# Kernel tuning notes

Hardware: AMD Instinct MI355X
Metric: run time of the kernel (lower is better)

Reference implementation:

```python
import jax, jax.numpy as jnp
import numpy as np
import math

B, L, H, NH = 8, 512, 512, 8
DH = H // NH


def setup_inputs() -> dict:
    key = jax.random.key(0)
    ks = jax.random.split(key, 12)
    src = jax.random.normal(ks[0], (B, L, H), dtype=jnp.float32)
    seq_len = jax.random.randint(ks[1], (B,), L // 2, L + 1).astype(jnp.int32)
    seq_len = seq_len.at[0].set(L)  # guarantee max(seq_len) == L
    pe = jax.random.normal(ks[2], (2 * L, H), dtype=jnp.float32) * 0.02
    s = 1.0 / math.sqrt(H)
    Wq = jax.random.normal(ks[3], (H, H), dtype=jnp.float32) * s
    bq = jnp.zeros((H,), jnp.float32)
    Wk = jax.random.normal(ks[4], (H, H), dtype=jnp.float32) * s
    bk = jnp.zeros((H,), jnp.float32)
    Wv = jax.random.normal(ks[5], (H, H), dtype=jnp.float32) * s
    bv = jnp.zeros((H,), jnp.float32)
    Wr = jax.random.normal(ks[6], (H, H), dtype=jnp.float32) * s
    br = jnp.zeros((H,), jnp.float32)
    u = jax.random.normal(ks[7], (NH, DH), dtype=jnp.float32) * 0.02
    v = jax.random.normal(ks[8], (NH, DH), dtype=jnp.float32) * 0.02
    gamma = jnp.ones((H,), jnp.float32)
    beta = jnp.zeros((H,), jnp.float32)
    return dict(src=src, seq_len=seq_len, pe=pe, Wq=Wq, bq=bq, Wk=Wk, bk=bk,
                Wv=Wv, bv=bv, Wr=Wr, br=br, u=u, v=v, gamma=gamma, beta=beta)


def reference(src, seq_len, pe, Wq, bq, Wk, bk, Wv, bv, Wr, br, u, v, gamma, beta):
    b, l, h = src.shape
    dh = h // NH
    # relative distance rel[i,j] = j - i, lookup pe[rel + L]  -> [L, L, H]
    rel = jnp.arange(l)[None, :] - jnp.arange(l)[:, None]
    R = pe[rel + l]
    # projections (torch Linear: y = x W^T + b)
    q = src @ Wq.T + bq
    k = src @ Wk.T + bk
    val = src @ Wv.T + bv
    R = R @ Wr.T + br
    # split heads
    q = q.reshape(b, l, NH, dh)
    k = k.reshape(b, l, NH, dh)
    val = val.reshape(b, l, NH, dh)
    R = R.reshape(l, l, NH, dh)
    # Transformer-XL score terms
    A = jnp.einsum('bihd,bjhd->bhij', q, k)
    Bt = jnp.einsum('bihd,ijhd->bhij', q, R)
    C = jnp.einsum('hd,bjhd->bhj', u, k)[:, :, None, :]
    D = jnp.einsum('ijhd,hd->hij', R, v)[None]
    scores = (A + Bt + C + D) / math.sqrt(dh)
    # key-side padding mask
    mask = jnp.arange(l)[None, :] < seq_len[:, None]  # [B, L]
    scores = jnp.where(mask[:, None, None, :], scores, jnp.float32(-1e15))
    attn = jax.nn.softmax(scores, axis=-1)
    out = jnp.einsum('bhij,bjhd->bihd', attn, val).reshape(b, l, h)
    res = src + out
    # LayerNorm (eps=1e-5) then exact GELU
    mu = jnp.mean(res, axis=-1, keepdims=True)
    var = jnp.mean((res - mu) ** 2, axis=-1, keepdims=True)
    ln = (res - mu) * jax.lax.rsqrt(var + 1e-5) * gamma + beta
    return jax.nn.gelu(ln, approximate=False)
```

## Files before the change

kernel.cpp:

```cpp
#include <hip/hip_runtime.h>
#include <math.h>

#define Bn 8
#define Ln 512
#define Hn 512
#define NHn 8
#define DHn 64

typedef __attribute__((ext_vector_type(8))) short short8;
typedef __attribute__((ext_vector_type(4))) float f32x4;

__device__ __forceinline__ unsigned short f2bf(float f) {
    unsigned int u = __float_as_uint(f);
    unsigned int r = (u + 0x7FFFu + ((u >> 16) & 1u)) >> 16;
    return (unsigned short)r;
}
__device__ __forceinline__ float bf2f(unsigned short s) {
    return __uint_as_float(((unsigned int)s) << 16);
}

__device__ __forceinline__ void gload16(const unsigned short* g, unsigned short* l) {
    __builtin_amdgcn_global_load_lds(
        (const __attribute__((address_space(1))) unsigned int*)g,
        (__attribute__((address_space(3))) unsigned int*)l, 16, 0, 0);
}

__global__ __launch_bounds__(256) void convert_kernel(
    const float* __restrict__ src, const float* __restrict__ pe,
    const float* __restrict__ Wq, const float* __restrict__ Wk,
    const float* __restrict__ Wv, const float* __restrict__ Wr,
    const float* __restrict__ bq, const float* __restrict__ bk,
    const float* __restrict__ bv,
    unsigned short* __restrict__ src_bf, unsigned short* __restrict__ pe_bf,
    unsigned short* __restrict__ Wcat_bf, unsigned short* __restrict__ Wr_bf,
    float* __restrict__ bcat)
{
    const int bid = blockIdx.x;
    const int tid = threadIdx.x;
    const float* in; unsigned short* outp; int base4;
    if (bid < 2048)      { in = src; outp = src_bf;           base4 = bid; }
    else if (bid < 2560) { in = pe;  outp = pe_bf;            base4 = bid - 2048; }
    else if (bid < 2816) { in = Wq;  outp = Wcat_bf;          base4 = bid - 2560; }
    else if (bid < 3072) { in = Wk;  outp = Wcat_bf + 262144; base4 = bid - 2816; }
    else if (bid < 3328) { in = Wv;  outp = Wcat_bf + 524288; base4 = bid - 3072; }
    else if (bid < 3584) { in = Wr;  outp = Wr_bf;            base4 = bid - 3328; }
    else {
        const int idx = (bid - 3584) * 256 + tid;
        if (idx < 512)            bcat[idx] = bq[idx];
        else if (idx < 1024)      bcat[idx] = bk[idx - 512];
        else if (idx < 1536)      bcat[idx] = bv[idx - 1024];
        return;
    }
    const int i4 = (base4 * 256 + tid) * 4;
    float4 x = *(const float4*)&in[i4];
    ushort4 o;
    o.x = f2bf(x.x); o.y = f2bf(x.y); o.z = f2bf(x.z); o.w = f2bf(x.w);
    *(ushort4*)&outp[i4] = o;
}

__global__ __launch_bounds__(256) void gemm_kernel(
    const unsigned short* __restrict__ src_bf,
    const unsigned short* __restrict__ Wcat_bf,
    const unsigned short* __restrict__ pe_bf,
    const unsigned short* __restrict__ Wr_bf,
    const float* __restrict__ bcat, const float* __restrict__ br,
    unsigned short* __restrict__ QKb,
    unsigned short* __restrict__ VTg,
    unsigned short* __restrict__ Rpb)
{
    const int bid = blockIdx.x;
    int mode, m0, n0;
    const unsigned short *A, *B;
    if (bid < 512) {
        mode = 0; m0 = (bid >> 3) * 64; n0 = (bid & 7) * 128;
        A = src_bf + (size_t)m0 * 512;
        B = Wcat_bf + (size_t)n0 * 512;
    } else if (bid < 768) {
        const int idx = bid - 512;
        mode = 1; m0 = (idx & 7) * 64; n0 = (idx >> 3) * 128;
        A = Wcat_bf + (size_t)(1024 + m0) * 512;
        B = src_bf + (size_t)n0 * 512;
    } else {
        const int idx = bid - 768;
        mode = 2; m0 = (idx >> 2) * 64; n0 = (idx & 3) * 128;
        A = pe_bf + (size_t)m0 * 512;
        B = Wr_bf + (size_t)n0 * 512;
    }

    __shared__ unsigned short lds[2][12288];

    const int t = threadIdx.x;
    const int wave = t >> 6, lane = t & 63;
    const int wm = (wave >> 1) * 32;
    const int wn = (wave & 1) * 64;
    const int l = lane & 15, g = lane >> 4;

    f32x4 acc[2][4] = {};

    const int lrow = lane >> 3;
    const int lcol = ((lane & 7) ^ lrow) * 8;
    const unsigned short* Ag0 = A + (size_t)((wave * 2 + 0) * 8 + lrow) * 512 + lcol;
    const unsigned short* Ag1 = A + (size_t)((wave * 2 + 1) * 8 + lrow) * 512 + lcol;
    const unsigned short* Bg0 = B + (size_t)((wave * 4 + 0) * 8 + lrow) * 512 + lcol;
    const unsigned short* Bg1 = B + (size_t)((wave * 4 + 1) * 8 + lrow) * 512 + lcol;
    const unsigned short* Bg2 = B + (size_t)((wave * 4 + 2) * 8 + lrow) * 512 + lcol;
    const unsigned short* Bg3 = B + (size_t)((wave * 4 + 3) * 8 + lrow) * 512 + lcol;

    const int aB0 = (wave * 2 + 0) * 512;
    const int aB1 = (wave * 2 + 1) * 512;
    const int bB0 = 4096 + (wave * 4 + 0) * 512;
    const int bB1 = 4096 + (wave * 4 + 1) * 512;
    const int bB2 = 4096 + (wave * 4 + 2) * 512;
    const int bB3 = 4096 + (wave * 4 + 3) * 512;

    #define STAGE(buf, k0)  do {                         \
        unsigned short* Lb = &lds[buf][0];               \
        gload16(Ag0 + (k0), Lb + aB0);                   \
        gload16(Ag1 + (k0), Lb + aB1);                   \
        gload16(Bg0 + (k0), Lb + bB0);                   \
        gload16(Bg1 + (k0), Lb + bB1);                   \
        gload16(Bg2 + (k0), Lb + bB2);                   \
        gload16(Bg3 + (k0), Lb + bB3);                   \
    } while (0)

    STAGE(0, 0);
    __syncthreads();

    const int colA = (g ^ (lane & 7)) * 8;

    for (int k0 = 0; k0 < 512; k0 += 64) {
        const int cur = (k0 >> 6) & 1;
        if (k0 + 64 < 512) STAGE(cur ^ 1, k0 + 64);

        const unsigned short* Asb = &lds[cur][0];
        const unsigned short* Bsb = &lds[cur][4096];
        #pragma unroll
        for (int kk = 0; kk < 2; ++kk) {
            const int cofs = colA ^ (kk * 32);
            short8 af[2], bf[4];
            #pragma unroll
            for (int mt = 0; mt < 2; ++mt)
                af[mt] = *(const short8*)&Asb[(wm + mt * 16 + l) * 64 + cofs];
            #pragma unroll
            for (int nt = 0; nt < 4; ++nt)
                bf[nt] = *(const short8*)&Bsb[(wn + nt * 16 + l) * 64 + cofs];
            #pragma unroll
            for (int mt = 0; mt < 2; ++mt)
                #pragma unroll
                for (int nt = 0; nt < 4; ++nt)
                    acc[mt][nt] = __builtin_amdgcn_mfma_f32_16x16x32_bf16(
                        af[mt], bf[nt], acc[mt][nt], 0, 0, 0);
        }

        if (k0 + 64 < 512) __syncthreads();
    }
    #undef STAGE

    const int crow = g * 4;
    const int ccol = l;
    if (mode == 0) {
        #pragma unroll
        for (int mt = 0; mt < 2; ++mt)
            #pragma unroll
            for (int nt = 0; nt < 4; ++nt) {
                const int n = n0 + wn + nt * 16 + ccol;
                const float bn = bcat[n];
                #pragma unroll
                for (int r = 0; r < 4; ++r) {
                    const int m = m0 + wm + mt * 16 + crow + r;
                    QKb[(size_t)m * 1024 + n] = f2bf(acc[mt][nt][r] + bn);
                }
            }
    } else if (mode == 1) {
        #pragma unroll
        for (int mt = 0; mt < 2; ++mt)
            #pragma unroll
            for (int nt = 0; nt < 4; ++nt) {
                const int n = n0 + wn + nt * 16 + ccol;
                #pragma unroll
                for (int r = 0; r < 4; ++r) {
                    const int dv = m0 + wm + mt * 16 + crow + r;
                    VTg[(size_t)dv * 4096 + n] = f2bf(acc[mt][nt][r] + bcat[1024 + dv]);
                }
            }
    } else {
        #pragma unroll
        for (int mt = 0; mt < 2; ++mt)
            #pragma unroll
            for (int nt = 0; nt < 4; ++nt) {
                const int n = n0 + wn + nt * 16 + ccol;
                const float bn = br[n];
                #pragma unroll
                for (int r = 0; r < 4; ++r) {
                    const int m = m0 + wm + mt * 16 + crow + r;
                    Rpb[(size_t)m * 512 + n] = f2bf(acc[mt][nt][r] + bn);
                }
            }
    }
}

#define PADK 72
__global__ __launch_bounds__(256) void attn_kernel(
    const unsigned short* __restrict__ QKb,
    const unsigned short* __restrict__ VTg,
    const unsigned short* __restrict__ Rpb,
    const float* __restrict__ u, const float* __restrict__ v,
    const int* __restrict__ seq_len, unsigned short* __restrict__ Ob)
{
    const int i0 = blockIdx.x * 64;
    const int h  = blockIdx.y;
    const int b  = blockIdx.z;
    const int slen = seq_len[b];
    const int njt = (slen + 63) >> 6;

    __shared__ unsigned short k_s [64 * PADK];
    __shared__ unsigned short vT_s[64 * PADK];
    __shared__ unsigned short rs_s[64 * PADK];
    __shared__ unsigned short p_s [64 * PADK];
    __shared__ unsigned short qrTT[128 * 72];

    const int t = threadIdx.x;
    const int wave = t >> 6, lane = t & 63;
    const int l = lane & 15, g = lane >> 4;

    short8 af_qu[2], af_qv[2];
    {
        const unsigned short* qrow =
            QKb + (size_t)(b * 512 + i0 + wave * 16 + l) * 1024 + h * 64;
        #pragma unroll
        for (int kk = 0; kk < 2; ++kk) {
            const int c = kk * 32 + g * 8;
            unsigned short q8[8];
            *(uint4*)q8 = *(const uint4*)(qrow + c);
            float4 u0 = *(const float4*)(u + h * 64 + c);
            float4 u1 = *(const float4*)(u + h * 64 + c + 4);
            float4 v0 = *(const float4*)(v + h * 64 + c);
            float4 v1 = *(const float4*)(v + h * 64 + c + 4);
            float uf[8] = {u0.x,u0.y,u0.z,u0.w,u1.x,u1.y,u1.z,u1.w};
            float vf[8] = {v0.x,v0.y,v0.z,v0.w,v1.x,v1.y,v1.z,v1.w};
            short8 qu, qv;
            #pragma unroll
            for (int e = 0; e < 8; ++e) {
                float qf = bf2f(q8[e]);
                qu[e] = (short)f2bf(qf + uf[e]);
                qv[e] = (short)f2bf(qf + vf[e]);
            }
            af_qu[kk] = qu; af_qv[kk] = qv;
        }
    }

    short8 ones8;
    #pragma unroll
    for (int e = 0; e < 8; ++e) ones8[e] = (short)0x3F80;

    f32x4 accO[4] = {};
    f32x4 accL = {};

    const int jr = t >> 2, c0 = (t & 3) * 16;

    auto btChunk = [&](int slot0) {
        #pragma unroll
        for (int nt8 = 0; nt8 < 4; ++nt8) {
            f32x4 a = {};
            #pragma unroll
            for (int kk = 0; kk < 2; ++kk) {
                short8 br8 = *(const short8*)&rs_s[(nt8 * 16 + l) * PADK + kk * 32 + g * 8];
                a = __builtin_amdgcn_mfma_f32_16x16x32_bf16(af_qv[kk], br8, a, 0, 0, 0);
            }
            const int sl = slot0 + nt8 * 16 + l;
            ushort4 w4;
            w4.x = f2bf(a[0]); w4.y = f2bf(a[1]); w4.z = f2bf(a[2]); w4.w = f2bf(a[3]);
            *(ushort4*)(qrTT + sl * 72 + wave * 16 + g * 4) = w4;
        }
    };

    const unsigned short* rpA = Rpb + (size_t)(448 - i0 + jr) * 512 + h * 64 + c0;
    uint4 rA0 = *(const uint4*)(rpA);
    uint4 rA1 = *(const uint4*)(rpA + 8);
    const unsigned short* kp0 = QKb + (size_t)(b * 512 + jr) * 1024 + 512 + h * 64 + c0;
    uint4 kc0 = *(const uint4*)(kp0), kc1 = *(const uint4*)(kp0 + 8);
    const unsigned short* vp0 = VTg + (size_t)(h * 64 + jr) * 4096 + b * 512 + c0;
    uint4 vc0 = *(const uint4*)(vp0), vc1 = *(const uint4*)(vp0 + 8);
    const unsigned short* rp0 = Rpb + (size_t)(512 - i0 + jr) * 512 + h * 64 + c0;
    uint4 rc0 = *(const uint4*)(rp0), rc1 = *(const uint4*)(rp0 + 8);

    *(uint4*)(rs_s + jr * PADK + c0)     = rA0;
    *(uint4*)(rs_s + jr * PADK + c0 + 8) = rA1;
    __syncthreads();
    btChunk((448 - i0) & 127);

    for (int jt = 0; jt < njt; ++jt) {
        const int j0 = jt * 64;
        __syncthreads();

        *(uint4*)(k_s  + jr * PADK + c0)     = kc0;
        *(uint4*)(k_s  + jr * PADK + c0 + 8) = kc1;
        *(uint4*)(vT_s + jr * PADK + c0)     = vc0;
        *(uint4*)(vT_s + jr * PADK + c0 + 8) = vc1;
        *(uint4*)(rs_s + jr * PADK + c0)     = rc0;
        *(uint4*)(rs_s + jr * PADK + c0 + 8) = rc1;
        __syncthreads();

        if (jt + 1 < njt) {
            const unsigned short* kp =
                QKb + (size_t)(b * 512 + j0 + 64 + jr) * 1024 + 512 + h * 64 + c0;
            kc0 = *(const uint4*)(kp); kc1 = *(const uint4*)(kp + 8);
            const unsigned short* vp =
                VTg + (size_t)(h * 64 + jr) * 4096 + b * 512 + j0 + 64 + c0;
            vc0 = *(const uint4*)(vp); vc1 = *(const uint4*)(vp + 8);
            const unsigned short* rp =
                Rpb + (size_t)(j0 + 64 - i0 + 512 + jr) * 512 + h * 64 + c0;
            rc0 = *(const uint4*)(rp); rc1 = *(const uint4*)(rp + 8);
        }

        btChunk((j0 - i0 + 512) & 127);

        f32x4 accA[4];
        #pragma unroll
        for (int nt = 0; nt < 4; ++nt) {
            f32x4 a = {};
            #pragma unroll
            for (int kk = 0; kk < 2; ++kk) {
                short8 bk8 = *(const short8*)&k_s[(nt * 16 + l) * PADK + kk * 32 + g * 8];
                a = __builtin_amdgcn_mfma_f32_16x16x32_bf16(af_qu[kk], bk8, a, 0, 0, 0);
            }
            accA[nt] = a;
        }

        #pragma unroll
        for (int nt = 0; nt < 4; ++nt) {
            const bool masked = (j0 + nt * 16 + l) >= slen;
            #pragma unroll
            for (int r = 0; r < 4; ++r) {
                const int il = wave * 16 + g * 4 + r;
                const int slot = (j0 + nt * 16 + l - i0 - il + 512) & 127;
                const float qr = bf2f(qrTT[slot * 72 + il]);
                const float pe_ = masked ? 0.f : __expf((accA[nt][r] + qr) * 0.125f);
                p_s[(wave * 16 + g * 4 + r) * PADK + nt * 16 + l] = f2bf(pe_);
            }
        }

        short8 pa[2];
        #pragma unroll
        for (int kk = 0; kk < 2; ++kk)
            pa[kk] = *(const short8*)&p_s[(wave * 16 + l) * PADK + kk * 32 + g * 8];

        #pragma unroll
        for (int kk = 0; kk < 2; ++kk)
            accL = __builtin_amdgcn_mfma_f32_16x16x32_bf16(pa[kk], ones8, accL, 0, 0, 0);

        #pragma unroll
        for (int nt = 0; nt < 4; ++nt) {
            #pragma unroll
            for (int kk = 0; kk < 2; ++kk) {
                short8 bv8 = *(const short8*)&vT_s[(nt * 16 + l) * PADK + kk * 32 + g * 8];
                accO[nt] = __builtin_amdgcn_mfma_f32_16x16x32_bf16(pa[kk], bv8, accO[nt], 0, 0, 0);
            }
        }
    }

    float inv[4];
    #pragma unroll
    for (int r = 0; r < 4; ++r) inv[r] = 1.0f / accL[r];
    #pragma unroll
    for (int nt = 0; nt < 4; ++nt)
        #pragma unroll
        for (int r = 0; r < 4; ++r)
            Ob[(size_t)(b * 512 + i0 + wave * 16 + g * 4 + r) * 512 + h * 64 + nt * 16 + l]
                = f2bf(accO[nt][r] * inv[r]);
}

__global__ __launch_bounds__(256) void ln_gelu_kernel(
    const float* __restrict__ src, const unsigned short* __restrict__ Ob,
    const float* __restrict__ gamma, const float* __restrict__ beta,
    float* __restrict__ out)
{
    const int row  = blockIdx.x * 4 + (threadIdx.x >> 6);
    const int lane = threadIdx.x & 63;
    const int c0   = lane * 8;
    const float* s = &src[(size_t)row * 512 + c0];
    float4 s0 = *(const float4*)(s);
    float4 s1 = *(const float4*)(s + 4);
    unsigned short o8[8];
    *(uint4*)o8 = *(const uint4*)(Ob + (size_t)row * 512 + c0);
    float x[8];
    x[0] = s0.x + bf2f(o8[0]); x[1] = s0.y + bf2f(o8[1]);
    x[2] = s0.z + bf2f(o8[2]); x[3] = s0.w + bf2f(o8[3]);
    x[4] = s1.x + bf2f(o8[4]); x[5] = s1.y + bf2f(o8[5]);
    x[6] = s1.z + bf2f(o8[6]); x[7] = s1.w + bf2f(o8[7]);
    float sum = 0.f;
    #pragma unroll
    for (int e = 0; e < 8; ++e) sum += x[e];
    #pragma unroll
    for (int off = 32; off >= 1; off >>= 1) sum += __shfl_xor(sum, off, 64);
    const float mean = sum * (1.0f / 512.0f);
    float var = 0.f;
    #pragma unroll
    for (int e = 0; e < 8; ++e) { float d = x[e] - mean; var += d * d; }
    #pragma unroll
    for (int off = 32; off >= 1; off >>= 1) var += __shfl_xor(var, off, 64);
    var *= (1.0f / 512.0f);
    const float inv = rsqrtf(var + 1e-5f);
    float4 g0 = *(const float4*)(gamma + c0);
    float4 g1 = *(const float4*)(gamma + c0 + 4);
    float4 b0 = *(const float4*)(beta + c0);
    float4 b1 = *(const float4*)(beta + c0 + 4);
    float gm[8] = {g0.x,g0.y,g0.z,g0.w,g1.x,g1.y,g1.z,g1.w};
    float bt[8] = {b0.x,b0.y,b0.z,b0.w,b1.x,b1.y,b1.z,b1.w};
    float r8[8];
    #pragma unroll
    for (int e = 0; e < 8; ++e) {
        float ln = (x[e] - mean) * inv * gm[e] + bt[e];
        r8[e] = 0.5f * ln * (1.0f + erff(ln * 0.70710678118654752f));
    }
    float* op = &out[(size_t)row * 512 + c0];
    *(float4*)(op)     = make_float4(r8[0], r8[1], r8[2], r8[3]);
    *(float4*)(op + 4) = make_float4(r8[4], r8[5], r8[6], r8[7]);
}

extern "C" void kernel_launch(void* const* d_in, const int* in_sizes, int n_in,
                              void* d_out, int out_size, void* d_ws, size_t ws_size,
                              hipStream_t stream)
{
    const float* src     = (const float*)d_in[0];
    const int*   seq_len = (const int*)  d_in[1];
    const float* pe      = (const float*)d_in[2];
    const float* Wq      = (const float*)d_in[3];
    const float* bq      = (const float*)d_in[4];
    const float* Wk      = (const float*)d_in[5];
    const float* bk      = (const float*)d_in[6];
    const float* Wv      = (const float*)d_in[7];
    const float* bv      = (const float*)d_in[8];
    const float* Wr      = (const float*)d_in[9];
    const float* br      = (const float*)d_in[10];
    const float* u       = (const float*)d_in[11];
    const float* v       = (const float*)d_in[12];
    const float* gamma   = (const float*)d_in[13];
    const float* beta    = (const float*)d_in[14];
    float* out = (float*)d_out;

    char* w = (char*)d_ws;
    unsigned short* QKb     = (unsigned short*)(w);
    unsigned short* VTg     = (unsigned short*)(w + 8388608);
    unsigned short* Rpb     = (unsigned short*)(w + 12582912);
    unsigned short* Ob      = (unsigned short*)(w + 13631488);
    unsigned short* src_bf  = (unsigned short*)(w + 17825792);
    unsigned short* pe_bf   = (unsigned short*)(w + 22020096);
    unsigned short* Wcat_bf = (unsigned short*)(w + 23068672);
    unsigned short* Wr_bf   = (unsigned short*)(w + 24641536);
    float*          bcat    = (float*)         (w + 25165824);

    convert_kernel<<<dim3(3590), 256, 0, stream>>>(
        src, pe, Wq, Wk, Wv, Wr, bq, bk, bv,
        src_bf, pe_bf, Wcat_bf, Wr_bf, bcat);

    gemm_kernel<<<dim3(832), 256, 0, stream>>>(
        src_bf, Wcat_bf, pe_bf, Wr_bf, bcat, br, QKb, VTg, Rpb);

    attn_kernel<<<dim3(8, NHn, Bn), 256, 0, stream>>>(QKb, VTg, Rpb, u, v, seq_len, Ob);

    ln_gelu_kernel<<<dim3(Bn * Ln / 4), 256, 0, stream>>>(src, Ob, gamma, beta, out);
}
```

Measured before the change: 131.6 us.

## Fuse all stages into one persistent kernel with grid-wide barriers

Merges the convert, GEMM, attention and LayerNorm/GELU kernels into a single persistent kernel of 512 blocks. The stages are separated by software global barriers built on atomic counters, and the barrier state is reset with a memset before launch. This removes the launch gaps between kernels and the per-launch overhead. In exchange, the GEMM and convert stages now loop over virtual blocks with less parallelism per pass, and the barriers spin on global atomics. Correctness depends on all 512 blocks being co-resident (launch bounds 256,2).

```diff
diff --git a/kernel.cpp b/kernel.cpp
--- a/kernel.cpp
+++ b/kernel.cpp
@@ -6,6 +6,7 @@
 #define Hn 512
 #define NHn 8
 #define DHn 64
+#define NBLK 512
 
 typedef __attribute__((ext_vector_type(8))) short short8;
 typedef __attribute__((ext_vector_type(4))) float f32x4;
@@ -18,404 +19,416 @@
 __device__ __forceinline__ float bf2f(unsigned short s) {
     return __uint_as_float(((unsigned int)s) << 16);
 }
-
 __device__ __forceinline__ void gload16(const unsigned short* g, unsigned short* l) {
     __builtin_amdgcn_global_load_lds(
         (const __attribute__((address_space(1))) unsigned int*)g,
         (__attribute__((address_space(3))) unsigned int*)l, 16, 0, 0);
 }
 
-__global__ __launch_bounds__(256) void convert_kernel(
-    const float* __restrict__ src, const float* __restrict__ pe,
-    const float* __restrict__ Wq, const float* __restrict__ Wk,
-    const float* __restrict__ Wv, const float* __restrict__ Wr,
-    const float* __restrict__ bq, const float* __restrict__ bk,
-    const float* __restrict__ bv,
+__device__ __forceinline__ void gbar(int* bar) {
+    __syncthreads();
+    if (threadIdx.x == 0) {
+        __threadfence();
+        int* cnt = bar;
+        int* gen = bar + 16;
+        const int g = __hip_atomic_load(gen, __ATOMIC_RELAXED, __HIP_MEMORY_SCOPE_AGENT);
+        const int a = __hip_atomic_fetch_add(cnt, 1, __ATOMIC_ACQ_REL, __HIP_MEMORY_SCOPE_AGENT);
+        if (a == NBLK - 1) {
+            __hip_atomic_store(cnt, 0, __ATOMIC_RELAXED, __HIP_MEMORY_SCOPE_AGENT);
+            __hip_atomic_fetch_add(gen, 1, __ATOMIC_RELEASE, __HIP_MEMORY_SCOPE_AGENT);
+        } else {
+            while (__hip_atomic_load(gen, __ATOMIC_RELAXED, __HIP_MEMORY_SCOPE_AGENT) == g)
+                __builtin_amdgcn_s_sleep(16);
+        }
+        __threadfence();
+    }
+    __syncthreads();
+}
+
+__global__ __launch_bounds__(256, 2) void mega_kernel(
+    const float* __restrict__ src, const int* __restrict__ seq_len,
+    const float* __restrict__ pe,
+    const float* __restrict__ Wq, const float* __restrict__ bq,
+    const float* __restrict__ Wk, const float* __restrict__ bk,
+    const float* __restrict__ Wv, const float* __restrict__ bv,
+    const float* __restrict__ Wr, const float* __restrict__ br,
+    const float* __restrict__ u, const float* __restrict__ v,
+    const float* __restrict__ gamma, const float* __restrict__ beta,
+    float* __restrict__ out,
+    unsigned short* __restrict__ QKb,
+    unsigned short* __restrict__ VTg,
+    unsigned short* __restrict__ Rpb,
+    unsigned short* __restrict__ Ob,
     unsigned short* __restrict__ src_bf, unsigned short* __restrict__ pe_bf,
     unsigned short* __restrict__ Wcat_bf, unsigned short* __restrict__ Wr_bf,
-    float* __restrict__ bcat)
+    float* __restrict__ bcat,
+    int* __restrict__ bar)
 {
-    const int bid = blockIdx.x;
-    const int tid = threadIdx.x;
-    const float* in; unsigned short* outp; int base4;
-    if (bid < 2048)      { in = src; outp = src_bf;           base4 = bid; }
-    else if (bid < 2560) { in = pe;  outp = pe_bf;            base4 = bid - 2048; }
-    else if (bid < 2816) { in = Wq;  outp = Wcat_bf;          base4 = bid - 2560; }
-    else if (bid < 3072) { in = Wk;  outp = Wcat_bf + 262144; base4 = bid - 2816; }
-    else if (bid < 3328) { in = Wv;  outp = Wcat_bf + 524288; base4 = bid - 3072; }
-    else if (bid < 3584) { in = Wr;  outp = Wr_bf;            base4 = bid - 3328; }
-    else {
-        const int idx = (bid - 3584) * 256 + tid;
-        if (idx < 512)            bcat[idx] = bq[idx];
-        else if (idx < 1024)      bcat[idx] = bk[idx - 512];
-        else if (idx < 1536)      bcat[idx] = bv[idx - 1024];
-        return;
+    __shared__ __align__(16) unsigned char smem_raw[55296];
+    const int t = threadIdx.x;
+
+    for (int vb = blockIdx.x; vb < 3590; vb += NBLK) {
+        if (vb >= 3584) {
+            const int idx = (vb - 3584) * 256 + t;
+            if (idx < 512)            bcat[idx] = bq[idx];
+            else if (idx < 1024)      bcat[idx] = bk[idx - 512];
+            else if (idx < 1536)      bcat[idx] = bv[idx - 1024];
+            continue;
+        }
+        const float* in; unsigned short* outp; int base4;
+        if (vb < 2048)      { in = src; outp = src_bf;           base4 = vb; }
+        else if (vb < 2560) { in = pe;  outp = pe_bf;            base4 = vb - 2048; }
+        else if (vb < 2816) { in = Wq;  outp = Wcat_bf;          base4 = vb - 2560; }
+        else if (vb < 3072) { in = Wk;  outp = Wcat_bf + 262144; base4 = vb - 2816; }
+        else if (vb < 3328) { in = Wv;  outp = Wcat_bf + 524288; base4 = vb - 3072; }
+        else                { in = Wr;  outp = Wr_bf;            base4 = vb - 3328; }
+        const int i4 = (base4 * 256 + t) * 4;
+        float4 x = *(const float4*)&in[i4];
+        ushort4 o;
+        o.x = f2bf(x.x); o.y = f2bf(x.y); o.z = f2bf(x.z); o.w = f2bf(x.w);
+        *(ushort4*)&outp[i4] = o;
     }
-    const int i4 = (base4 * 256 + tid) * 4;
-    float4 x = *(const float4*)&in[i4];
-    ushort4 o;
-    o.x = f2bf(x.x); o.y = f2bf(x.y); o.z = f2bf(x.z); o.w = f2bf(x.w);
-    *(ushort4*)&outp[i4] = o;
-}
-
-__global__ __launch_bounds__(256) void gemm_kernel(
-    const unsigned short* __restrict__ src_bf,
-    const unsigned short* __restrict__ Wcat_bf,
-    const unsigned short* __restrict__ pe_bf,
-    const unsigned short* __restrict__ Wr_bf,
-    const float* __restrict__ bcat, const float* __restrict__ br,
-    unsigned short* __restrict__ QKb,
-    unsigned short* __restrict__ VTg,
-    unsigned short* __restrict__ Rpb)
-{
-    const int bid = blockIdx.x;
-    int mode, m0, n0;
-    const unsigned short *A, *B;
-    if (bid < 512) {
-        mode = 0; m0 = (bid >> 3) * 64; n0 = (bid & 7) * 128;
-        A = src_bf + (size_t)m0 * 512;
-        B = Wcat_bf + (size_t)n0 * 512;
-    } else if (bid < 768) {
-        const int idx = bid - 512;
-        mode = 1; m0 = (idx & 7) * 64; n0 = (idx >> 3) * 128;
-        A = Wcat_bf + (size_t)(1024 + m0) * 512;
-        B = src_bf + (size_t)n0 * 512;
-    } else {
-        const int idx = bid - 768;
-        mode = 2; m0 = (idx >> 2) * 64; n0 = (idx & 3) * 128;
-        A = pe_bf + (size_t)m0 * 512;
-        B = Wr_bf + (size_t)n0 * 512;
+
+    gbar(bar);
+
+    {
+        unsigned short* lds0 = (unsigned short*)smem_raw;
+        unsigned short* lds1 = lds0 + 12288;
+        const int wave = t >> 6, lane = t & 63;
+        const int wm = (wave >> 1) * 32;
+        const int wn = (wave & 1) * 64;
+        const int l = lane & 15, g = lane >> 4;
+        const int lrow = lane >> 3;
+        const int lcol = ((lane & 7) ^ lrow) * 8;
+        const int colA = (g ^ (lane & 7)) * 8;
+        const int aB0 = (wave * 2 + 0) * 512;
+        const int aB1 = (wave * 2 + 1) * 512;
+        const int bB0 = 4096 + (wave * 4 + 0) * 512;
+        const int bB1 = 4096 + (wave * 4 + 1) * 512;
+        const int bB2 = 4096 + (wave * 4 + 2) * 512;
+        const int bB3 = 4096 + (wave * 4 + 3) * 512;
+
+        for (int vb = blockIdx.x; vb < 832; vb += NBLK) {
+            int mode, m0, n0;
+            const unsigned short *A, *B;
+            if (vb < 512) {
+                mode = 0; m0 = (vb >> 3) * 64; n0 = (vb & 7) * 128;
+                A = src_bf + (size_t)m0 * 512;
+                B = Wcat_bf + (size_t)n0 * 512;
+            } else if (vb < 768) {
+                const int idx = vb - 512;
+                mode = 1; m0 = (idx & 7) * 64; n0 = (idx >> 3) * 128;
+                A = Wcat_bf + (size_t)(1024 + m0) * 512;
+                B = src_bf + (size_t)n0 * 512;
+            } else {
+                const int idx = vb - 768;
+                mode = 2; m0 = (idx >> 2) * 64; n0 = (idx & 3) * 128;
+                A = pe_bf + (size_t)m0 * 512;
+                B = Wr_bf + (size_t)n0 * 512;
+            }
+            const unsigned short* Ag0 = A + (size_t)((wave * 2 + 0) * 8 + lrow) * 512 + lcol;
+            const unsigned short* Ag1 = A + (size_t)((wave * 2 + 1) * 8 + lrow) * 512 + lcol;
+            const unsigned short* Bg0 = B + (size_t)((wave * 4 + 0) * 8 + lrow) * 512 + lcol;
+            const unsigned short* Bg1 = B + (size_t)((wave * 4 + 1) * 8 + lrow) * 512 + lcol;
+            const unsigned short* Bg2 = B + (size_t)((wave * 4 + 2) * 8 + lrow) * 512 + lcol;
+            const unsigned short* Bg3 = B + (size_t)((wave * 4 + 3) * 8 + lrow) * 512 + lcol;
+
+            auto stage = [&](unsigned short* Lb, int k0) {
+                gload16(Ag0 + k0, Lb + aB0);
+                gload16(Ag1 + k0, Lb + aB1);
+                gload16(Bg0 + k0, Lb + bB0);
+                gload16(Bg1 + k0, Lb + bB1);
+                gload16(Bg2 + k0, Lb + bB2);
+                gload16(Bg3 + k0, Lb + bB3);
+            };
+
+            f32x4 acc[2][4] = {};
+            stage(lds0, 0);
+            __syncthreads();
+
+            for (int k0 = 0; k0 < 512; k0 += 64) {
+                unsigned short* curb = ((k0 >> 6) & 1) ? lds1 : lds0;
+                unsigned short* nxtb = ((k0 >> 6) & 1) ? lds0 : lds1;
+                if (k0 + 64 < 512) stage(nxtb, k0 + 64);
+
+                const unsigned short* Asb = curb;
+                const unsigned short* Bsb = curb + 4096;
+                #pragma unroll
+                for (int kk = 0; kk < 2; ++kk) {
+                    const int cofs = colA ^ (kk * 32);
+                    short8 af[2], bf[4];
+                    #pragma unroll
+                    for (int mt = 0; mt < 2; ++mt)
+                        af[mt] = *(const short8*)&Asb[(wm + mt * 16 + l) * 64 + cofs];
+                    #pragma unroll
+                    for (int nt = 0; nt < 4; ++nt)
+                        bf[nt] = *(const short8*)&Bsb[(wn + nt * 16 + l) * 64 + cofs];
+                    #pragma unroll
+                    for (int mt = 0; mt < 2; ++mt)
+                        #pragma unroll
+                        for (int nt = 0; nt < 4; ++nt)
+                            acc[mt][nt] = __builtin_amdgcn_mfma_f32_16x16x32_bf16(
+                                af[mt], bf[nt], acc[mt][nt], 0, 0, 0);
+                }
+                if (k0 + 64 < 512) __syncthreads();
+            }
+
+            const int crow = g * 4, ccol = l;
+            if (mode == 0) {
+                #pragma unroll
+                for (int mt = 0; mt < 2; ++mt)
+                    #pragma unroll
+                    for (int nt = 0; nt < 4; ++nt) {
+                        const int n = n0 + wn + nt * 16 + ccol;
+                        const float bn = bcat[n];
+                        #pragma unroll
+                        for (int r = 0; r < 4; ++r) {
+                            const int m = m0 + wm + mt * 16 + crow + r;
+                            QKb[(size_t)m * 1024 + n] = f2bf(acc[mt][nt][r] + bn);
+                        }
+                    }
+            } else if (mode == 1) {
+                #pragma unroll
+                for (int mt = 0; mt < 2; ++mt)
+                    #pragma unroll
+                    for (int nt = 0; nt < 4; ++nt) {
+                        const int n = n0 + wn + nt * 16 + ccol;
+                        #pragma unroll
+                        for (int r = 0; r < 4; ++r) {
+                            const int dv = m0 + wm + mt * 16 + crow + r;
+                            VTg[(size_t)dv * 4096 + n] = f2bf(acc[mt][nt][r] + bcat[1024 + dv]);
+                        }
+                    }
+            } else {
+                #pragma unroll
+                for (int mt = 0; mt < 2; ++mt)
+                    #pragma unroll
+                    for (int nt = 0; nt < 4; ++nt) {
+                        const int n = n0 + wn + nt * 16 + ccol;
+                        const float bn = br[n];
+                        #pragma unroll
+                        for (int r = 0; r < 4; ++r) {
+                            const int m = m0 + wm + mt * 16 + crow + r;
+                            Rpb[(size_t)m * 512 + n] = f2bf(acc[mt][nt][r] + bn);
+                        }
+                    }
+            }
+        }
     }
 
-    __shared__ unsigned short lds[2][12288];
-
-    const int t = threadIdx.x;
-    const int wave = t >> 6, lane = t & 63;
-    const int wm = (wave >> 1) * 32;
-    const int wn = (wave & 1) * 64;
-    const int l = lane & 15, g = lane >> 4;
-
-    f32x4 acc[2][4] = {};
-
-    const int lrow = lane >> 3;
-    const int lcol = ((lane & 7) ^ lrow) * 8;
-    const unsigned short* Ag0 = A + (size_t)((wave * 2 + 0) * 8 + lrow) * 512 + lcol;
-    const unsigned short* Ag1 = A + (size_t)((wave * 2 + 1) * 8 + lrow) * 512 + lcol;
-    const unsigned short* Bg0 = B + (size_t)((wave * 4 + 0) * 8 + lrow) * 512 + lcol;
-    const unsigned short* Bg1 = B + (size_t)((wave * 4 + 1) * 8 + lrow) * 512 + lcol;
-    const unsigned short* Bg2 = B + (size_t)((wave * 4 + 2) * 8 + lrow) * 512 + lcol;
-    const unsigned short* Bg3 = B + (size_t)((wave * 4 + 3) * 8 + lrow) * 512 + lcol;
-
-    const int aB0 = (wave * 2 + 0) * 512;
-    const int aB1 = (wave * 2 + 1) * 512;
-    const int bB0 = 4096 + (wave * 4 + 0) * 512;
-    const int bB1 = 4096 + (wave * 4 + 1) * 512;
-    const int bB2 = 4096 + (wave * 4 + 2) * 512;
-    const int bB3 = 4096 + (wave * 4 + 3) * 512;
-
-    #define STAGE(buf, k0)  do {                         \
-        unsigned short* Lb = &lds[buf][0];               \
-        gload16(Ag0 + (k0), Lb + aB0);                   \
-        gload16(Ag1 + (k0), Lb + aB1);                   \
-        gload16(Bg0 + (k0), Lb + bB0);                   \
-        gload16(Bg1 + (k0), Lb + bB1);                   \
-        gload16(Bg2 + (k0), Lb + bB2);                   \
-        gload16(Bg3 + (k0), Lb + bB3);                   \
-    } while (0)
-
-    STAGE(0, 0);
-    __syncthreads();
-
-    const int colA = (g ^ (lane & 7)) * 8;
-
-    for (int k0 = 0; k0 < 512; k0 += 64) {
-        const int cur = (k0 >> 6) & 1;
-        if (k0 + 64 < 512) STAGE(cur ^ 1, k0 + 64);
-
-        const unsigned short* Asb = &lds[cur][0];
-        const unsigned short* Bsb = &lds[cur][4096];
-        #pragma unroll
-        for (int kk = 0; kk < 2; ++kk) {
-            const int cofs = colA ^ (kk * 32);
-            short8 af[2], bf[4];
-            #pragma unroll
-            for (int mt = 0; mt < 2; ++mt)
-                af[mt] = *(const short8*)&Asb[(wm + mt * 16 + l) * 64 + cofs];
-            #pragma unroll
-            for (int nt = 0; nt < 4; ++nt)
-                bf[nt] = *(const short8*)&Bsb[(wn + nt * 16 + l) * 64 + cofs];
-            #pragma unroll
-            for (int mt = 0; mt < 2; ++mt)
-                #pragma unroll
-                for (int nt = 0; nt < 4; ++nt)
-                    acc[mt][nt] = __builtin_amdgcn_mfma_f32_16x16x32_bf16(
-                        af[mt], bf[nt], acc[mt][nt], 0, 0, 0);
-        }
-
-        if (k0 + 64 < 512) __syncthreads();
+    gbar(bar);
+
+    {
+        #define PADK 72
+        unsigned short* k_s  = (unsigned short*)smem_raw;
+        unsigned short* vT_s = k_s  + 64 * PADK;
+        unsigned short* rs_s = vT_s + 64 * PADK;
+        unsigned short* p_s  = rs_s + 64 * PADK;
+        unsigned short* qrTT = p_s  + 64 * PADK;
+
+        const int vb = blockIdx.x;
+        const int i0 = (vb & 7) * 64;
+        const int h  = (vb >> 3) & 7;
+        const int b  = vb >> 6;
+        const int slen = seq_len[b];
+        const int njt = (slen + 63) >> 6;
+
+        const int wave = t >> 6, lane = t & 63;
+        const int l = lane & 15, g = lane >> 4;
+
+        short8 af_qu[2], af_qv[2];
+        {
+            const unsigned short* qrow =
+                QKb + (size_t)(b * 512 + i0 + wave * 16 + l) * 1024 + h * 64;
+            #pragma unroll
+            for (int kk = 0; kk < 2; ++kk) {
+                const int c = kk * 32 + g * 8;
+                unsigned short q8[8];
+                *(uint4*)q8 = *(const uint4*)(qrow + c);
+                float4 u0 = *(const float4*)(u + h * 64 + c);
+                float4 u1 = *(const float4*)(u + h * 64 + c + 4);
+                float4 v0 = *(const float4*)(v + h * 64 + c);
+                float4 v1 = *(const float4*)(v + h * 64 + c + 4);
+                float uf[8] = {u0.x,u0.y,u0.z,u0.w,u1.x,u1.y,u1.z,u1.w};
+                float vf[8] = {v0.x,v0.y,v0.z,v0.w,v1.x,v1.y,v1.z,v1.w};
+                short8 qu, qv;
+                #pragma unroll
+                for (int e = 0; e < 8; ++e) {
+                    float qf = bf2f(q8[e]);
+                    qu[e] = (short)f2bf(qf + uf[e]);
+                    qv[e] = (short)f2bf(qf + vf[e]);
+                }
+                af_qu[kk] = qu; af_qv[kk] = qv;
+            }
+        }
+
+        short8 ones8;
+        #pragma unroll
+        for (int e = 0; e < 8; ++e) ones8[e] = (short)0x3F80;
+
+        f32x4 accO[4] = {};
+        f32x4 accL = {};
+
+        const int jr = t >> 2, c0 = (t & 3) * 16;
+
+        auto btChunk = [&](int slot0) {
+            #pragma unroll
+            for (int nt8 = 0; nt8 < 4; ++nt8) {
+                f32x4 a = {};
+                #pragma unroll
+                for (int kk = 0; kk < 2; ++kk) {
+                    short8 br8 = *(const short8*)&rs_s[(nt8 * 16 + l) * PADK + kk * 32 + g * 8];
+                    a = __builtin_amdgcn_mfma_f32_16x16x32_bf16(af_qv[kk], br8, a, 0, 0, 0);
+                }
+                const int sl = slot0 + nt8 * 16 + l;
+                ushort4 w4;
+                w4.x = f2bf(a[0]); w4.y = f2bf(a[1]); w4.z = f2bf(a[2]); w4.w = f2bf(a[3]);
+                *(ushort4*)(qrTT + sl * 72 + wave * 16 + g * 4) = w4;
+            }
+        };
+
+        const unsigned short* rpA = Rpb + (size_t)(448 - i0 + jr) * 512 + h * 64 + c0;
+        uint4 rA0 = *(const uint4*)(rpA);
+        uint4 rA1 = *(const uint4*)(rpA + 8);
+        const unsigned short* kp0 = QKb + (size_t)(b * 512 + jr) * 1024 + 512 + h * 64 + c0;
+        uint4 kc0 = *(const uint4*)(kp0), kc1 = *(const uint4*)(kp0 + 8);
+        const unsigned short* vp0 = VTg + (size_t)(h * 64 + jr) * 4096 + b * 512 + c0;
+        uint4 vc0 = *(const uint4*)(vp0), vc1 = *(const uint4*)(vp0 + 8);
+        const unsigned short* rp0 = Rpb + (size_t)(512 - i0 + jr) * 512 + h * 64 + c0;
+        uint4 rc0 = *(const uint4*)(rp0), rc1 = *(const uint4*)(rp0 + 8);
+
+        *(uint4*)(rs_s + jr * PADK + c0)     = rA0;
+        *(uint4*)(rs_s + jr * PADK + c0 + 8) = rA1;
+        __syncthreads();
+        btChunk((448 - i0) & 127);
+
+        for (int jt = 0; jt < njt; ++jt) {
+            const int j0 = jt * 64;
+            __syncthreads();
+
+            *(uint4*)(k_s  + jr * PADK + c0)     = kc0;
+            *(uint4*)(k_s  + jr * PADK + c0 + 8) = kc1;
+            *(uint4*)(vT_s + jr * PADK + c0)     = vc0;
+            *(uint4*)(vT_s + jr * PADK + c0 + 8) = vc1;
+            *(uint4*)(rs_s + jr * PADK + c0)     = rc0;
+            *(uint4*)(rs_s + jr * PADK + c0 + 8) = rc1;
+            __syncthreads();
+
+            if (jt + 1 < njt) {
+                const unsigned short* kp =
+                    QKb + (size_t)(b * 512 + j0 + 64 + jr) * 1024 + 512 + h * 64 + c0;
+                kc0 = *(const uint4*)(kp); kc1 = *(const uint4*)(kp + 8);
+                const unsigned short* vp =
+                    VTg + (size_t)(h * 64 + jr) * 4096 + b * 512 + j0 + 64 + c0;
+                vc0 = *(const uint4*)(vp); vc1 = *(const uint4*)(vp + 8);
+                const unsigned short* rp =
+                    Rpb + (size_t)(j0 + 64 - i0 + 512 + jr) * 512 + h * 64 + c0;
+                rc0 = *(const uint4*)(rp); rc1 = *(const uint4*)(rp + 8);
+            }
+
+            btChunk((j0 - i0 + 512) & 127);
+
+            f32x4 accA[4];
+            #pragma unroll
+            for (int nt = 0; nt < 4; ++nt) {
+                f32x4 a = {};
+                #pragma unroll
+                for (int kk = 0; kk < 2; ++kk) {
+                    short8 bk8 = *(const short8*)&k_s[(nt * 16 + l) * PADK + kk * 32 + g * 8];
+                    a = __builtin_amdgcn_mfma_f32_16x16x32_bf16(af_qu[kk], bk8, a, 0, 0, 0);
+                }
+                accA[nt] = a;
+            }
+
+            #pragma unroll
+            for (int nt = 0; nt < 4; ++nt) {
+                const bool masked = (j0 + nt * 16 + l) >= slen;
+                #pragma unroll
+                for (int r = 0; r < 4; ++r) {
+                    const int il = wave * 16 + g * 4 + r;
+                    const int slot = (j0 + nt * 16 + l - i0 - il + 512) & 127;
+                    const float qr = bf2f(qrTT[slot * 72 + il]);
+                    const float pe_ = masked ? 0.f : __expf((accA[nt][r] + qr) * 0.125f);
+                    p_s[(wave * 16 + g * 4 + r) * PADK + nt * 16 + l] = f2bf(pe_);
+                }
+            }
+
+            short8 pa[2];
+            #pragma unroll
+            for (int kk = 0; kk < 2; ++kk)
+                pa[kk] = *(const short8*)&p_s[(wave * 16 + l) * PADK + kk * 32 + g * 8];
+
+            #pragma unroll
+            for (int kk = 0; kk < 2; ++kk)
+                accL = __builtin_amdgcn_mfma_f32_16x16x32_bf16(pa[kk], ones8, accL, 0, 0, 0);
+
+            #pragma unroll
+            for (int nt = 0; nt < 4; ++nt) {
+                #pragma unroll
+                for (int kk = 0; kk < 2; ++kk) {
+                    short8 bv8 = *(const short8*)&vT_s[(nt * 16 + l) * PADK + kk * 32 + g * 8];
+                    accO[nt] = __builtin_amdgcn_mfma_f32_16x16x32_bf16(pa[kk], bv8, accO[nt], 0, 0, 0);
+                }
+            }
+        }
+
+        float inv[4];
+        #pragma unroll
+        for (int r = 0; r < 4; ++r) inv[r] = 1.0f / accL[r];
+        #pragma unroll
+        for (int nt = 0; nt < 4; ++nt)
+            #pragma unroll
+            for (int r = 0; r < 4; ++r)
+                Ob[(size_t)(b * 512 + i0 + wave * 16 + g * 4 + r) * 512 + h * 64 + nt * 16 + l]
+                    = f2bf(accO[nt][r] * inv[r]);
+        #undef PADK
     }
-    #undef STAGE
-
-    const int crow = g * 4;
-    const int ccol = l;
-    if (mode == 0) {
-        #pragma unroll
-        for (int mt = 0; mt < 2; ++mt)
-            #pragma unroll
-            for (int nt = 0; nt < 4; ++nt) {
-                const int n = n0 + wn + nt * 16 + ccol;
-                const float bn = bcat[n];
-                #pragma unroll
-                for (int r = 0; r < 4; ++r) {
-                    const int m = m0 + wm + mt * 16 + crow + r;
-                    QKb[(size_t)m * 1024 + n] = f2bf(acc[mt][nt][r] + bn);
-                }
-            }
-    } else if (mode == 1) {
-        #pragma unroll
-        for (int mt = 0; mt < 2; ++mt)
-            #pragma unroll
-            for (int nt = 0; nt < 4; ++nt) {
-                const int n = n0 + wn + nt * 16 + ccol;
-                #pragma unroll
-                for (int r = 0; r < 4; ++r) {
-                    const int dv = m0 + wm + mt * 16 + crow + r;
-                    VTg[(size_t)dv * 4096 + n] = f2bf(acc[mt][nt][r] + bcat[1024 + dv]);
-                }
-            }
-    } else {
-        #pragma unroll
-        for (int mt = 0; mt < 2; ++mt)
-            #pragma unroll
-            for (int nt = 0; nt < 4; ++nt) {
-                const int n = n0 + wn + nt * 16 + ccol;
-                const float bn = br[n];
-                #pragma unroll
-                for (int r = 0; r < 4; ++r) {
-                    const int m = m0 + wm + mt * 16 + crow + r;
-                    Rpb[(size_t)m * 512 + n] = f2bf(acc[mt][nt][r] + bn);
-                }
-            }
+
+    gbar(bar);
+
+    for (int vb = blockIdx.x; vb < 1024; vb += NBLK) {
+        const int row  = vb * 4 + (t >> 6);
+        const int lane = t & 63;
+        const int c0   = lane * 8;
+        const float* s = &src[(size_t)row * 512 + c0];
+        float4 s0 = *(const float4*)(s);
+        float4 s1 = *(const float4*)(s + 4);
+        unsigned short o8[8];
+        *(uint4*)o8 = *(const uint4*)(Ob + (size_t)row * 512 + c0);
+        float x[8];
+        x[0] = s0.x + bf2f(o8[0]); x[1] = s0.y + bf2f(o8[1]);
+        x[2] = s0.z + bf2f(o8[2]); x[3] = s0.w + bf2f(o8[3]);
+        x[4] = s1.x + bf2f(o8[4]); x[5] = s1.y + bf2f(o8[5]);
+        x[6] = s1.z + bf2f(o8[6]); x[7] = s1.w + bf2f(o8[7]);
+        float sum = 0.f;
+        #pragma unroll
+        for (int e = 0; e < 8; ++e) sum += x[e];
+        #pragma unroll
+        for (int off = 32; off >= 1; off >>= 1) sum += __shfl_xor(sum, off, 64);
+        const float mean = sum * (1.0f / 512.0f);
+        float var = 0.f;
+        #pragma unroll
+        for (int e = 0; e < 8; ++e) { float d = x[e] - mean; var += d * d; }
+        #pragma unroll
+        for (int off = 32; off >= 1; off >>= 1) var += __shfl_xor(var, off, 64);
+        var *= (1.0f / 512.0f);
+        const float invs = rsqrtf(var + 1e-5f);
+        float4 g0 = *(const float4*)(gamma + c0);
+        float4 g1 = *(const float4*)(gamma + c0 + 4);
+        float4 b0 = *(const float4*)(beta + c0);
+        float4 b1 = *(const float4*)(beta + c0 + 4);
+        float gm[8] = {g0.x,g0.y,g0.z,g0.w,g1.x,g1.y,g1.z,g1.w};
+        float bt[8] = {b0.x,b0.y,b0.z,b0.w,b1.x,b1.y,b1.z,b1.w};
+        float r8[8];
+        #pragma unroll
+        for (int e = 0; e < 8; ++e) {
+            float ln = (x[e] - mean) * invs * gm[e] + bt[e];
+            r8[e] = 0.5f * ln * (1.0f + erff(ln * 0.70710678118654752f));
+        }
+        float* op = &out[(size_t)row * 512 + c0];
+        *(float4*)(op)     = make_float4(r8[0], r8[1], r8[2], r8[3]);
+        *(float4*)(op + 4) = make_float4(r8[4], r8[5], r8[6], r8[7]);
     }
-}
-
-#define PADK 72
-__global__ __launch_bounds__(256) void attn_kernel(
-    const unsigned short* __restrict__ QKb,
-    const unsigned short* __restrict__ VTg,
-    const unsigned short* __restrict__ Rpb,
-    const float* __restrict__ u, const float* __restrict__ v,
-    const int* __restrict__ seq_len, unsigned short* __restrict__ Ob)
-{
-    const int i0 = blockIdx.x * 64;
-    const int h  = blockIdx.y;
-    const int b  = blockIdx.z;
-    const int slen = seq_len[b];
-    const int njt = (slen + 63) >> 6;
-
-    __shared__ unsigned short k_s [64 * PADK];
-    __shared__ unsigned short vT_s[64 * PADK];
-    __shared__ unsigned short rs_s[64 * PADK];
-    __shared__ unsigned short p_s [64 * PADK];
-    __shared__ unsigned short qrTT[128 * 72];
-
-    const int t = threadIdx.x;
-    const int wave = t >> 6, lane = t & 63;
-    const int l = lane & 15, g = lane >> 4;
-
-    short8 af_qu[2], af_qv[2];
-    {
-        const unsigned short* qrow =
-            QKb + (size_t)(b * 512 + i0 + wave * 16 + l) * 1024 + h * 64;
-        #pragma unroll
-        for (int kk = 0; kk < 2; ++kk) {
-            const int c = kk * 32 + g * 8;
-            unsigned short q8[8];
-            *(uint4*)q8 = *(const uint4*)(qrow + c);
-            float4 u0 = *(const float4*)(u + h * 64 + c);
-            float4 u1 = *(const float4*)(u + h * 64 + c + 4);
-            float4 v0 = *(const float4*)(v + h * 64 + c);
-            float4 v1 = *(const float4*)(v + h * 64 + c + 4);
-            float uf[8] = {u0.x,u0.y,u0.z,u0.w,u1.x,u1.y,u1.z,u1.w};
-            float vf[8] = {v0.x,v0.y,v0.z,v0.w,v1.x,v1.y,v1.z,v1.w};
-            short8 qu, qv;
-            #pragma unroll
-            for (int e = 0; e < 8; ++e) {
-                float qf = bf2f(q8[e]);
-                qu[e] = (short)f2bf(qf + uf[e]);
-                qv[e] = (short)f2bf(qf + vf[e]);
-            }
-            af_qu[kk] = qu; af_qv[kk] = qv;
-        }
-    }
-
-    short8 ones8;
-    #pragma unroll
-    for (int e = 0; e < 8; ++e) ones8[e] = (short)0x3F80;
-
-    f32x4 accO[4] = {};
-    f32x4 accL = {};
-
-    const int jr = t >> 2, c0 = (t & 3) * 16;
-
-    auto btChunk = [&](int slot0) {
-        #pragma unroll
-        for (int nt8 = 0; nt8 < 4; ++nt8) {
-            f32x4 a = {};
-            #pragma unroll
-            for (int kk = 0; kk < 2; ++kk) {
-                short8 br8 = *(const short8*)&rs_s[(nt8 * 16 + l) * PADK + kk * 32 + g * 8];
-                a = __builtin_amdgcn_mfma_f32_16x16x32_bf16(af_qv[kk], br8, a, 0, 0, 0);
-            }
-            const int sl = slot0 + nt8 * 16 + l;
-            ushort4 w4;
-            w4.x = f2bf(a[0]); w4.y = f2bf(a[1]); w4.z = f2bf(a[2]); w4.w = f2bf(a[3]);
-            *(ushort4*)(qrTT + sl * 72 + wave * 16 + g * 4) = w4;
-        }
-    };
-
-    const unsigned short* rpA = Rpb + (size_t)(448 - i0 + jr) * 512 + h * 64 + c0;
-    uint4 rA0 = *(const uint4*)(rpA);
-    uint4 rA1 = *(const uint4*)(rpA + 8);
-    const unsigned short* kp0 = QKb + (size_t)(b * 512 + jr) * 1024 + 512 + h * 64 + c0;
-    uint4 kc0 = *(const uint4*)(kp0), kc1 = *(const uint4*)(kp0 + 8);
-    const unsigned short* vp0 = VTg + (size_t)(h * 64 + jr) * 4096 + b * 512 + c0;
-    uint4 vc0 = *(const uint4*)(vp0), vc1 = *(const uint4*)(vp0 + 8);
-    const unsigned short* rp0 = Rpb + (size_t)(512 - i0 + jr) * 512 + h * 64 + c0;
-    uint4 rc0 = *(const uint4*)(rp0), rc1 = *(const uint4*)(rp0 + 8);
-
-    *(uint4*)(rs_s + jr * PADK + c0)     = rA0;
-    *(uint4*)(rs_s + jr * PADK + c0 + 8) = rA1;
-    __syncthreads();
-    btChunk((448 - i0) & 127);
-
-    for (int jt = 0; jt < njt; ++jt) {
-        const int j0 = jt * 64;
-        __syncthreads();
-
-        *(uint4*)(k_s  + jr * PADK + c0)     = kc0;
-        *(uint4*)(k_s  + jr * PADK + c0 + 8) = kc1;
-        *(uint4*)(vT_s + jr * PADK + c0)     = vc0;
-        *(uint4*)(vT_s + jr * PADK + c0 + 8) = vc1;
-        *(uint4*)(rs_s + jr * PADK + c0)     = rc0;
-        *(uint4*)(rs_s + jr * PADK + c0 + 8) = rc1;
-        __syncthreads();
-
-        if (jt + 1 < njt) {
-            const unsigned short* kp =
-                QKb + (size_t)(b * 512 + j0 + 64 + jr) * 1024 + 512 + h * 64 + c0;
-            kc0 = *(const uint4*)(kp); kc1 = *(const uint4*)(kp + 8);
-            const unsigned short* vp =
-                VTg + (size_t)(h * 64 + jr) * 4096 + b * 512 + j0 + 64 + c0;
-            vc0 = *(const uint4*)(vp); vc1 = *(const uint4*)(vp + 8);
-            const unsigned short* rp =
-                Rpb + (size_t)(j0 + 64 - i0 + 512 + jr) * 512 + h * 64 + c0;
-            rc0 = *(const uint4*)(rp); rc1 = *(const uint4*)(rp + 8);
-        }
-
-        btChunk((j0 - i0 + 512) & 127);
-
-        f32x4 accA[4];
-        #pragma unroll
-        for (int nt = 0; nt < 4; ++nt) {
-            f32x4 a = {};
-            #pragma unroll
-            for (int kk = 0; kk < 2; ++kk) {
-                short8 bk8 = *(const short8*)&k_s[(nt * 16 + l) * PADK + kk * 32 + g * 8];
-                a = __builtin_amdgcn_mfma_f32_16x16x32_bf16(af_qu[kk], bk8, a, 0, 0, 0);
-            }
-            accA[nt] = a;
-        }
-
-        #pragma unroll
-        for (int nt = 0; nt < 4; ++nt) {
-            const bool masked = (j0 + nt * 16 + l) >= slen;
-            #pragma unroll
-            for (int r = 0; r < 4; ++r) {
-                const int il = wave * 16 + g * 4 + r;
-                const int slot = (j0 + nt * 16 + l - i0 - il + 512) & 127;
-                const float qr = bf2f(qrTT[slot * 72 + il]);
-                const float pe_ = masked ? 0.f : __expf((accA[nt][r] + qr) * 0.125f);
-                p_s[(wave * 16 + g * 4 + r) * PADK + nt * 16 + l] = f2bf(pe_);
-            }
-        }
-
-        short8 pa[2];
-        #pragma unroll
-        for (int kk = 0; kk < 2; ++kk)
-            pa[kk] = *(const short8*)&p_s[(wave * 16 + l) * PADK + kk * 32 + g * 8];
-
-        #pragma unroll
-        for (int kk = 0; kk < 2; ++kk)
-            accL = __builtin_amdgcn_mfma_f32_16x16x32_bf16(pa[kk], ones8, accL, 0, 0, 0);
-
-        #pragma unroll
-        for (int nt = 0; nt < 4; ++nt) {
-            #pragma unroll
-            for (int kk = 0; kk < 2; ++kk) {
-                short8 bv8 = *(const short8*)&vT_s[(nt * 16 + l) * PADK + kk * 32 + g * 8];
-                accO[nt] = __builtin_amdgcn_mfma_f32_16x16x32_bf16(pa[kk], bv8, accO[nt], 0, 0, 0);
-            }
-        }
-    }
-
-    float inv[4];
-    #pragma unroll
-    for (int r = 0; r < 4; ++r) inv[r] = 1.0f / accL[r];
-    #pragma unroll
-    for (int nt = 0; nt < 4; ++nt)
-        #pragma unroll
-        for (int r = 0; r < 4; ++r)
-            Ob[(size_t)(b * 512 + i0 + wave * 16 + g * 4 + r) * 512 + h * 64 + nt * 16 + l]
-                = f2bf(accO[nt][r] * inv[r]);
-}
-
-__global__ __launch_bounds__(256) void ln_gelu_kernel(
-    const float* __restrict__ src, const unsigned short* __restrict__ Ob,
-    const float* __restrict__ gamma, const float* __restrict__ beta,
-    float* __restrict__ out)
-{
-    const int row  = blockIdx.x * 4 + (threadIdx.x >> 6);
-    const int lane = threadIdx.x & 63;
-    const int c0   = lane * 8;
-    const float* s = &src[(size_t)row * 512 + c0];
-    float4 s0 = *(const float4*)(s);
-    float4 s1 = *(const float4*)(s + 4);
-    unsigned short o8[8];
-    *(uint4*)o8 = *(const uint4*)(Ob + (size_t)row * 512 + c0);
-    float x[8];
-    x[0] = s0.x + bf2f(o8[0]); x[1] = s0.y + bf2f(o8[1]);
-    x[2] = s0.z + bf2f(o8[2]); x[3] = s0.w + bf2f(o8[3]);
-    x[4] = s1.x + bf2f(o8[4]); x[5] = s1.y + bf2f(o8[5]);
-    x[6] = s1.z + bf2f(o8[6]); x[7] = s1.w + bf2f(o8[7]);
-    float sum = 0.f;
-    #pragma unroll
-    for (int e = 0; e < 8; ++e) sum += x[e];
-    #pragma unroll
-    for (int off = 32; off >= 1; off >>= 1) sum += __shfl_xor(sum, off, 64);
-    const float mean = sum * (1.0f / 512.0f);
-    float var = 0.f;
-    #pragma unroll
-    for (int e = 0; e < 8; ++e) { float d = x[e] - mean; var += d * d; }
-    #pragma unroll
-    for (int off = 32; off >= 1; off >>= 1) var += __shfl_xor(var, off, 64);
-    var *= (1.0f / 512.0f);
-    const float inv = rsqrtf(var + 1e-5f);
-    float4 g0 = *(const float4*)(gamma + c0);
-    float4 g1 = *(const float4*)(gamma + c0 + 4);
-    float4 b0 = *(const float4*)(beta + c0);
-    float4 b1 = *(const float4*)(beta + c0 + 4);
-    float gm[8] = {g0.x,g0.y,g0.z,g0.w,g1.x,g1.y,g1.z,g1.w};
-    float bt[8] = {b0.x,b0.y,b0.z,b0.w,b1.x,b1.y,b1.z,b1.w};
-    float r8[8];
-    #pragma unroll
-    for (int e = 0; e < 8; ++e) {
-        float ln = (x[e] - mean) * inv * gm[e] + bt[e];
-        r8[e] = 0.5f * ln * (1.0f + erff(ln * 0.70710678118654752f));
-    }
-    float* op = &out[(size_t)row * 512 + c0];
-    *(float4*)(op)     = make_float4(r8[0], r8[1], r8[2], r8[3]);
-    *(float4*)(op + 4) = make_float4(r8[4], r8[5], r8[6], r8[7]);
 }
 
 extern "C" void kernel_launch(void* const* d_in, const int* in_sizes, int n_in,
@@ -449,15 +462,11 @@
     unsigned short* Wcat_bf = (unsigned short*)(w + 23068672);
     unsigned short* Wr_bf   = (unsigned short*)(w + 24641536);
     float*          bcat    = (float*)         (w + 25165824);
-
-    convert_kernel<<<dim3(3590), 256, 0, stream>>>(
-        src, pe, Wq, Wk, Wv, Wr, bq, bk, bv,
-        src_bf, pe_bf, Wcat_bf, Wr_bf, bcat);
-
-    gemm_kernel<<<dim3(832), 256, 0, stream>>>(
-        src_bf, Wcat_bf, pe_bf, Wr_bf, bcat, br, QKb, VTg, Rpb);
-
-    attn_kernel<<<dim3(8, NHn, Bn), 256, 0, stream>>>(QKb, VTg, Rpb, u, v, seq_len, Ob);
-
-    ln_gelu_kernel<<<dim3(Bn * Ln / 4), 256, 0, stream>>>(src, Ob, gamma, beta, out);
-}
+    int*            bar     = (int*)           (w + 25174016);
+
+    hipMemsetAsync(bar, 0, 128, stream);
+
+    mega_kernel<<<dim3(NBLK), 256, 0, stream>>>(
+        src, seq_len, pe, Wq, bq, Wk, bk, Wv, bv, Wr, br, u, v, gamma, beta, out,
+        QKb, VTg, Rpb, Ob, src_bf, pe_bf, Wcat_bf, Wr_bf, bcat, bar);
+}
```

Measured after the change: 337.7 us. 157% more time.
